# Kernel tuning notes

Measured on AMD Instinct MI355X. Metric: run time of the kernel, lower is better.

The kernel has to match this reference:

```python
import jax, jax.numpy as jnp
import numpy as np

N = 524288          # query points
N_COMP = 36         # sdf_n_comp
GRID = 512          # cubic grid resolution
SDF_DIM = 256
APP_DIM = 128
MAT_MODE = [(0, 1), (0, 2), (1, 2)]
VEC_MODE = [2, 1, 0]
PE_FREQS = (1.0, 2.0, 4.0)  # sdf_multires=3, log-sampled 2^0..2^2


def _pos_enc(x):
    # NeRF embedder, include_input=True: [x, sin(f x), cos(f x) per freq]
    outs = [x]
    for f in PE_FREQS:
        outs.append(jnp.sin(x * f))
        outs.append(jnp.cos(x * f))
    return jnp.concatenate(outs, axis=-1)  # (N, 21)


def _bilinear_plane(plane, gx, gy):
    # plane: (C, H, W); gx indexes W, gy indexes H; align_corners=True
    C, H, W = plane.shape
    px = (gx + 1.0) * 0.5 * (W - 1)
    py = (gy + 1.0) * 0.5 * (H - 1)
    x0 = jnp.clip(jnp.floor(px), 0, W - 2).astype(jnp.int32)
    y0 = jnp.clip(jnp.floor(py), 0, H - 2).astype(jnp.int32)
    x1, y1 = x0 + 1, y0 + 1
    wx = px - x0
    wy = py - y0
    f00 = plane[:, y0, x0]  # (C, N)
    f01 = plane[:, y0, x1]
    f10 = plane[:, y1, x0]
    f11 = plane[:, y1, x1]
    return (f00 * (1 - wx) + f01 * wx) * (1 - wy) + (f10 * (1 - wx) + f11 * wx) * wy


def _linear_line(line, g):
    # line: (C, L); g in [-1, 1]; align_corners=True
    C, L = line.shape
    p = (g + 1.0) * 0.5 * (L - 1)
    i0 = jnp.clip(jnp.floor(p), 0, L - 2).astype(jnp.int32)
    w = p - i0
    return line[:, i0] * (1 - w) + line[:, i0 + 1] * w  # (C, N)


def setup_inputs() -> dict:
    key = jax.random.key(0)
    ks = jax.random.split(key, 6)
    xyz = jax.random.uniform(ks[0], (N, 3), dtype=jnp.float32)  # points in aabb [0,1]^3
    planes = jax.random.normal(ks[1], (3, N_COMP, GRID, GRID), dtype=jnp.float32) * 0.1
    lines = jax.random.normal(ks[2], (3, N_COMP, GRID), dtype=jnp.float32) * 0.1
    in_ch = N_COMP * 3 + 21  # 129
    W1 = jax.random.normal(ks[3], (in_ch, SDF_DIM), dtype=jnp.float32) * (np.sqrt(2.0) / np.sqrt(SDF_DIM))
    b1 = jnp.zeros((SDF_DIM,), dtype=jnp.float32)
    W2 = jax.random.normal(ks[4], (SDF_DIM, 1 + APP_DIM), dtype=jnp.float32) * 0.0001 + np.sqrt(np.pi) / np.sqrt(SDF_DIM)
    b2 = jnp.full((1 + APP_DIM,), -0.2, dtype=jnp.float32)  # init_radius bias
    return {"xyz": xyz, "planes": planes, "lines": lines, "W1": W1, "b1": b1, "W2": W2, "b2": b2}


def reference(xyz, planes, lines, W1, b1, W2, b2):
    # contraction: normalize aabb [0,1]^3 -> [-1,1]
    xn = 2.0 * xyz - 1.0  # (N, 3)
    # sampling coords are detached in the original (coordinate_plane.detach())
    xs = jax.lax.stop_gradient(xn)
    feats = []
    for i in range(3):
        m0, m1 = MAT_MODE[i]
        pfeat = _bilinear_plane(planes[i], xs[:, m0], xs[:, m1])  # (C, N)
        lfeat = _linear_line(lines[i], xs[:, VEC_MODE[i]])        # (C, N)
        feats.append(pfeat * lfeat)
    feat = jnp.concatenate(feats, axis=0).T  # (N, 3C)
    pe = _pos_enc(xn)                         # (N, 21)
    h = jnp.concatenate([feat, pe], axis=-1)  # (N, 129)
    h = jax.nn.softplus(100.0 * (h @ W1 + b1)) / 100.0  # Softplus(beta=100)
    out = h @ W2 + b2  # (N, 1 + app_dim); out[..., :1] is the SDF
    return out
```

## Files before the change

kernel.cpp:

```cpp
#include <hip/hip_runtime.h>
#include <math.h>

typedef unsigned short u16;
typedef unsigned int u32;
typedef __attribute__((ext_vector_type(2))) u32 u32x2;
typedef __attribute__((ext_vector_type(8))) short short8;
typedef __attribute__((ext_vector_type(4))) float f32x4;
typedef __attribute__((ext_vector_type(2))) float f32x2;

#define OFF_LINES_T 62914560u
#define OFF_W1S     63037440u
#define OFF_W2S     63119360u
#define WS_NEEDED   63217664u

__device__ __forceinline__ float bf_lo(u32 u){ union{u32 i;float f;} v; v.i = u << 16; return v.f; }
__device__ __forceinline__ float bf_hi(u32 u){ union{u32 i;float f;} v; v.i = u & 0xffff0000u; return v.f; }
__device__ __forceinline__ u16 f2bf(float f){ union{float f;u32 i;} v; v.f=f; u32 i=v.i; return (u16)((i + 0x7fffu + ((i>>16)&1u)) >> 16); }
__device__ __forceinline__ u32 pack2bf(float lo, float hi){ return (u32)f2bf(lo) | ((u32)f2bf(hi)<<16); }
__device__ __forceinline__ u32 pack2bf_fast(float lo, float hi){
  return __builtin_amdgcn_perm(__float_as_uint(hi) + 0x8000u,
                               __float_as_uint(lo) + 0x8000u, 0x07060302u);
}
__device__ __forceinline__ u16 f2bf_fast(float f){ return (u16)((__float_as_uint(f) + 0x8000u) >> 16); }

__device__ __forceinline__ int map_k1(int kp){
  if (kp < 120){ int g = kp/40, r = kp - g*40; return (r<36) ? g*36 + r : -1; }
  if (kp < 141) return kp - 12;
  return -1;
}

#define NB_TP 3072
#define NB_TL 6
#define NB_W1 20
#define NB_W2 24
__global__ void k_pre(const float* __restrict__ planes, const float* __restrict__ lines,
                      const float* __restrict__ W1, const float* __restrict__ W2,
                      u16* __restrict__ pt, u16* __restrict__ lt,
                      u16* __restrict__ w1s, u16* __restrict__ w2s){
  const int b = blockIdx.x;
  const int tid = threadIdx.x;
  if (b < NB_TP){
    int t = b*256 + tid;
    int i = t >> 18;
    int yx = t & 262143;
    const float* src = planes + (size_t)i*9437184 + yx;
    uint4* dst = reinterpret_cast<uint4*>(pt + (size_t)t*40);
#pragma unroll
    for (int cc=0; cc<5; cc++){
      float v[8];
#pragma unroll
      for (int e=0;e<8;e++){
        int c = cc*8+e;
        v[e] = (c<36) ? src[(size_t)c*262144] : 0.f;
      }
      uint4 o; o.x=pack2bf(v[0],v[1]); o.y=pack2bf(v[2],v[3]); o.z=pack2bf(v[4],v[5]); o.w=pack2bf(v[6],v[7]);
      dst[cc]=o;
    }
  } else if (b < NB_TP+NB_TL){
    int t = (b-NB_TP)*256 + tid;
    int i = t >> 9, g = t & 511;
    const float* src = lines + (size_t)i*18432 + g;
    uint4* dst = reinterpret_cast<uint4*>(lt + (size_t)t*40);
#pragma unroll
    for (int cc=0; cc<5; cc++){
      float v[8];
#pragma unroll
      for (int e=0;e<8;e++){
        int c = cc*8+e;
        v[e] = (c<36) ? src[(size_t)c*512] : 0.f;
      }
      uint4 o; o.x=pack2bf(v[0],v[1]); o.y=pack2bf(v[2],v[3]); o.z=pack2bf(v[4],v[5]); o.w=pack2bf(v[6],v[7]);
      dst[cc]=o;
    }
  } else if (b < NB_TP+NB_TL+NB_W1){
    int t = (b-(NB_TP+NB_TL))*256 + tid;
    int lane = t & 63;
    int fid = t >> 6;
    int nt = fid/5, kt = fid - nt*5;
    int n = nt*16 + (lane & 15);
    int kb = kt*32 + (lane >> 4)*8;
    float v[8];
#pragma unroll
    for (int j=0;j<8;j++){ int k = map_k1(kb+j); v[j] = (k>=0) ? W1[k*256+n] : 0.f; }
    uint4 o; o.x=pack2bf(v[0],v[1]); o.y=pack2bf(v[2],v[3]); o.z=pack2bf(v[4],v[5]); o.w=pack2bf(v[6],v[7]);
    *reinterpret_cast<uint4*>(w1s + (size_t)t*8) = o;
  } else {
    int t = (b-(NB_TP+NB_TL+NB_W1))*256 + tid;
    int lane = t & 63;
    int fid = t >> 6;
    int kb = (fid & 7)*32 + (lane >> 4)*8;
    int n = (fid >> 3)*16 + (lane & 15);
    float v[8];
#pragma unroll
    for (int j=0;j<8;j++){ int k = kb+j; v[j] = (n<129) ? W2[k*129+n] : 0.f; }
    uint4 o; o.x=pack2bf(v[0],v[1]); o.y=pack2bf(v[2],v[3]); o.z=pack2bf(v[4],v[5]); o.w=pack2bf(v[6],v[7]);
    *reinterpret_cast<uint4*>(w2s + (size_t)t*8) = o;
  }
}

__device__ __forceinline__ f32x2 bfx2(u32 u){
  f32x2 r;
  r.x = __uint_as_float(u << 16);
  r.y = __uint_as_float(u & 0xffff0000u);
  return r;
}

__device__ __forceinline__ u32 blend2(u32 u00,u32 u01,u32 u10,u32 u11,u32 g0,u32 g1,
                                      float w00,float w01,float w10,float w11,
                                      float v0,float v1){
  f32x2 pf = bfx2(u00)*w00 + bfx2(u01)*w01 + bfx2(u10)*w10 + bfx2(u11)*w11;
  f32x2 lf = bfx2(g0)*v0 + bfx2(g1)*v1;
  f32x2 r  = pf*lf;
  return pack2bf_fast(r.x, r.y);
}

#define FSTRIDE 168
#define HSTRIDE 264

__global__ void __launch_bounds__(512, 4) k_main(
    const float* __restrict__ xyz, const u16* __restrict__ pt,
    const u16* __restrict__ lt, const u16* __restrict__ w1s,
    const u16* __restrict__ w2s, const float* __restrict__ b1,
    const float* __restrict__ b2, float* __restrict__ out)
{
  __shared__ u16 smem[64*HSTRIDE];
  const int tid = threadIdx.x;
  const int p = tid >> 3, q = tid & 7;
  const int gp = blockIdx.x*64 + p;
  const float u0 = xyz[gp*3], u1 = xyz[gp*3+1], u2 = xyz[gp*3+2];
  const float xn0 = 2.f*u0-1.f, xn1 = 2.f*u1-1.f, xn2 = 2.f*u2-1.f;

  if (q < 6){
    const int i = q >> 1, part = q & 1;
    float gxv, gyv, gzv;
    if      (i==0){ gxv=xn0; gyv=xn1; gzv=xn2; }
    else if (i==1){ gxv=xn0; gyv=xn2; gzv=xn1; }
    else          { gxv=xn1; gyv=xn2; gzv=xn0; }
    float px=(gxv+1.0f)*0.5f*511.0f, py=(gyv+1.0f)*0.5f*511.0f, pz=(gzv+1.0f)*0.5f*511.0f;
    float fx=fminf(fmaxf(floorf(px),0.f),510.f);
    float fy=fminf(fmaxf(floorf(py),0.f),510.f);
    float fz=fminf(fmaxf(floorf(pz),0.f),510.f);
    int ix=(int)fx, iy=(int)fy, iz=(int)fz;
    float wx=px-fx, wy=py-fy, wz=pz-fz;
    const float cwx = 1.f-wx, cwy = 1.f-wy;
    const float w00 = cwx*cwy, w01 = wx*cwy, w10 = cwx*wy, w11 = wx*wy;
    const float v0 = 1.f-wz, v1 = wz;
    const u16* base  = pt + (size_t)((i<<18)+(iy<<9)+ix)*40 + part*20;
    const u16* lbase = lt + (size_t)((i<<9)+iz)*40 + part*20;

    u32x2 A00[5],A01[5],A10[5],A11[5],E0[5],E1[5];
#pragma unroll
    for (int c=0; c<5; c++){
      A00[c] = *reinterpret_cast<const u32x2*>(base + c*4);
      A01[c] = *reinterpret_cast<const u32x2*>(base + 40 + c*4);
      A10[c] = *reinterpret_cast<const u32x2*>(base + 20480 + c*4);
      A11[c] = *reinterpret_cast<const u32x2*>(base + 20520 + c*4);
      E0[c]  = *reinterpret_cast<const u32x2*>(lbase + c*4);
      E1[c]  = *reinterpret_cast<const u32x2*>(lbase + 40 + c*4);
    }
    u16* dst = smem + p*FSTRIDE + i*40 + part*20;
#pragma unroll
    for (int c=0; c<5; c++){
      u32x2 o;
      o.x = blend2(A00[c].x,A01[c].x,A10[c].x,A11[c].x,E0[c].x,E1[c].x, w00,w01,w10,w11,v0,v1);
      o.y = blend2(A00[c].y,A01[c].y,A10[c].y,A11[c].y,E0[c].y,E1[c].y, w00,w01,w10,w11,v0,v1);
      *reinterpret_cast<u32x2*>(dst + c*4) = o;
    }
  } else if (q == 6){
    float v[20];
    v[0]=xn0; v[1]=xn1; v[2]=xn2;
    v[3]=__sinf(xn0);      v[4]=__sinf(xn1);      v[5]=__sinf(xn2);
    v[6]=__cosf(xn0);      v[7]=__cosf(xn1);      v[8]=__cosf(xn2);
    v[9]=__sinf(2.f*xn0);  v[10]=__sinf(2.f*xn1); v[11]=__sinf(2.f*xn2);
    v[12]=__cosf(2.f*xn0); v[13]=__cosf(2.f*xn1); v[14]=__cosf(2.f*xn2);
    v[15]=__sinf(4.f*xn0); v[16]=__sinf(4.f*xn1); v[17]=__sinf(4.f*xn2);
    v[18]=__cosf(4.f*xn0); v[19]=__cosf(4.f*xn1);
    u16* dst = smem + p*FSTRIDE + 120;
#pragma unroll
    for (int c=0; c<10; c++)
      *reinterpret_cast<u32*>(dst + c*2) = pack2bf_fast(v[c*2], v[c*2+1]);
  } else {
    u16* dst = smem + p*FSTRIDE + 140;
    *reinterpret_cast<u32*>(dst) = pack2bf_fast(__cosf(4.f*xn2), 0.f);
#pragma unroll
    for (int c=1; c<10; c++)
      *reinterpret_cast<u32*>(dst + c*2) = 0u;
  }
  __syncthreads();

  const int lane = tid & 63;
  const int w = tid >> 6;
  const int wm = w & 1, wn = w >> 1;
  const int lm = lane & 15;
  const int quad = lane >> 4;
  const f32x4 zero = {0.f,0.f,0.f,0.f};
  f32x4 acc1[2][4];
#pragma unroll
  for (int mt=0; mt<2; mt++)
#pragma unroll
    for (int nt=0; nt<4; nt++) acc1[mt][nt] = zero;

#pragma unroll
  for (int kt=0; kt<5; kt++){
    short8 a[2];
#pragma unroll
    for (int mt=0; mt<2; mt++)
      a[mt] = *reinterpret_cast<const short8*>(smem + ((wm*2+mt)*16 + lm)*FSTRIDE + kt*32 + quad*8);
    short8 b[4];
#pragma unroll
    for (int nt=0; nt<4; nt++)
      b[nt] = *reinterpret_cast<const short8*>(w1s + (size_t)(((wn*4+nt)*5 + kt)*64 + lane)*8);
#pragma unroll
    for (int mt=0; mt<2; mt++)
#pragma unroll
      for (int nt=0; nt<4; nt++)
        acc1[mt][nt] = __builtin_amdgcn_mfma_f32_16x16x32_bf16(a[mt], b[nt], acc1[mt][nt], 0,0,0);
  }
  __syncthreads();

#pragma unroll
  for (int nt=0; nt<4; nt++){
    int col = wn*64 + nt*16 + lm;
    float bias = b1[col];
#pragma unroll
    for (int mt=0; mt<2; mt++){
#pragma unroll
      for (int r=0; r<4; r++){
        float xv = acc1[mt][nt][r] + bias;
        float z = 100.f*xv;
        float y = (z > 15.f) ? xv : __logf(1.f + __expf(z))*0.01f;
        int row = (wm*2+mt)*16 + quad*4 + r;
        smem[row*HSTRIDE + col] = f2bf_fast(y);
      }
    }
  }
  __syncthreads();

  f32x4 acc2[2][3];
#pragma unroll
  for (int mt=0; mt<2; mt++)
#pragma unroll
    for (int nt=0; nt<3; nt++) acc2[mt][nt] = zero;

#pragma unroll
  for (int kt=0; kt<8; kt++){
    short8 a[2];
#pragma unroll
    for (int mt=0; mt<2; mt++)
      a[mt] = *reinterpret_cast<const short8*>(smem + ((wm*2+mt)*16 + lm)*HSTRIDE + kt*32 + quad*8);
    short8 b[3];
#pragma unroll
    for (int nt=0; nt<3; nt++){
      int ntg = wn*3 + nt;
      b[nt] = *reinterpret_cast<const short8*>(w2s + (size_t)((ntg*8 + kt)*64 + lane)*8);
    }
#pragma unroll
    for (int mt=0; mt<2; mt++)
#pragma unroll
      for (int nt=0; nt<3; nt++)
        acc2[mt][nt] = __builtin_amdgcn_mfma_f32_16x16x32_bf16(a[mt], b[nt], acc2[mt][nt], 0,0,0);
  }

#pragma unroll
  for (int nt=0; nt<3; nt++){
    int j = (wn*3 + nt)*16 + lm;
    if (j < 129){
      float bias = b2[j];
#pragma unroll
      for (int mt=0; mt<2; mt++){
#pragma unroll
        for (int r=0; r<4; r++){
          int row = (wm*2+mt)*16 + quad*4 + r;
          __builtin_nontemporal_store(acc2[mt][nt][r] + bias,
                                      &out[(size_t)(blockIdx.x*64 + row)*129 + j]);
        }
      }
    }
  }
}

extern "C" void kernel_launch(void* const* d_in, const int* in_sizes, int n_in,
                              void* d_out, int out_size, void* d_ws, size_t ws_size,
                              hipStream_t stream) {
  const float* xyz    = (const float*)d_in[0];
  const float* planes = (const float*)d_in[1];
  const float* lines  = (const float*)d_in[2];
  const float* W1     = (const float*)d_in[3];
  const float* b1     = (const float*)d_in[4];
  const float* W2     = (const float*)d_in[5];
  const float* b2     = (const float*)d_in[6];
  if (ws_size < (size_t)WS_NEEDED) return;

  u16* pt  = (u16*)((char*)d_ws);
  u16* lt  = (u16*)((char*)d_ws + OFF_LINES_T);
  u16* w1s = (u16*)((char*)d_ws + OFF_W1S);
  u16* w2s = (u16*)((char*)d_ws + OFF_W2S);

  k_pre<<<NB_TP+NB_TL+NB_W1+NB_W2, 256, 0, stream>>>(planes, lines, W1, W2, pt, lt, w1s, w2s);
  k_main<<<8192, 512, 0, stream>>>(xyz, pt, lt, w1s, w2s, b1, b2, (float*)d_out);
}
```

Before: 673.1 us.

## Raise occupancy to five blocks, widen gather loads, reuse accumulator registers

Measured after the change: 646.2 us. 4.0% less time.

```diff
diff --git a/kernel.cpp b/kernel.cpp
--- a/kernel.cpp
+++ b/kernel.cpp
@@ -117,7 +117,7 @@
 #define FSTRIDE 168
 #define HSTRIDE 264
 
-__global__ void __launch_bounds__(512, 4) k_main(
+__global__ void __launch_bounds__(512, 5) k_main(
     const float* __restrict__ xyz, const u16* __restrict__ pt,
     const u16* __restrict__ lt, const u16* __restrict__ w1s,
     const u16* __restrict__ w2s, const float* __restrict__ b1,
@@ -145,26 +145,26 @@
     const float cwx = 1.f-wx, cwy = 1.f-wy;
     const float w00 = cwx*cwy, w01 = wx*cwy, w10 = cwx*wy, w11 = wx*wy;
     const float v0 = 1.f-wz, v1 = wz;
-    const u16* base  = pt + (size_t)((i<<18)+(iy<<9)+ix)*40 + part*20;
-    const u16* lbase = lt + (size_t)((i<<9)+iz)*40 + part*20;
-
-    u32x2 A00[5],A01[5],A10[5],A11[5],E0[5],E1[5];
-#pragma unroll
-    for (int c=0; c<5; c++){
-      A00[c] = *reinterpret_cast<const u32x2*>(base + c*4);
-      A01[c] = *reinterpret_cast<const u32x2*>(base + 40 + c*4);
-      A10[c] = *reinterpret_cast<const u32x2*>(base + 20480 + c*4);
-      A11[c] = *reinterpret_cast<const u32x2*>(base + 20520 + c*4);
-      E0[c]  = *reinterpret_cast<const u32x2*>(lbase + c*4);
-      E1[c]  = *reinterpret_cast<const u32x2*>(lbase + 40 + c*4);
-    }
-    u16* dst = smem + p*FSTRIDE + i*40 + part*20;
-#pragma unroll
-    for (int c=0; c<5; c++){
-      u32x2 o;
-      o.x = blend2(A00[c].x,A01[c].x,A10[c].x,A11[c].x,E0[c].x,E1[c].x, w00,w01,w10,w11,v0,v1);
-      o.y = blend2(A00[c].y,A01[c].y,A10[c].y,A11[c].y,E0[c].y,E1[c].y, w00,w01,w10,w11,v0,v1);
-      *reinterpret_cast<u32x2*>(dst + c*4) = o;
+    const int nch = part ? 2 : 3;
+    const u16* tb = pt + (size_t)((i<<18)+(iy<<9)+ix)*40 + part*24;
+    const u16* lb = lt + (size_t)((i<<9)+iz)*40 + part*24;
+    u16* dst = smem + p*FSTRIDE + i*40 + part*24;
+#pragma unroll
+    for (int ch=0; ch<3; ch++){
+      if (ch < nch){
+        uint4 a00 = *reinterpret_cast<const uint4*>(tb + ch*8);
+        uint4 a01 = *reinterpret_cast<const uint4*>(tb + 40 + ch*8);
+        uint4 a10 = *reinterpret_cast<const uint4*>(tb + 20480 + ch*8);
+        uint4 a11 = *reinterpret_cast<const uint4*>(tb + 20520 + ch*8);
+        uint4 e0  = *reinterpret_cast<const uint4*>(lb + ch*8);
+        uint4 e1  = *reinterpret_cast<const uint4*>(lb + 40 + ch*8);
+        uint4 o;
+        o.x = blend2(a00.x,a01.x,a10.x,a11.x,e0.x,e1.x, w00,w01,w10,w11,v0,v1);
+        o.y = blend2(a00.y,a01.y,a10.y,a11.y,e0.y,e1.y, w00,w01,w10,w11,v0,v1);
+        o.z = blend2(a00.z,a01.z,a10.z,a11.z,e0.z,e1.z, w00,w01,w10,w11,v0,v1);
+        o.w = blend2(a00.w,a01.w,a10.w,a11.w,e0.w,e1.w, w00,w01,w10,w11,v0,v1);
+        *reinterpret_cast<uint4*>(dst + ch*8) = o;
+      }
     }
   } else if (q == 6){
     float v[20];
@@ -194,11 +194,11 @@
   const int lm = lane & 15;
   const int quad = lane >> 4;
   const f32x4 zero = {0.f,0.f,0.f,0.f};
-  f32x4 acc1[2][4];
+  f32x4 acc[2][4];
 #pragma unroll
   for (int mt=0; mt<2; mt++)
 #pragma unroll
-    for (int nt=0; nt<4; nt++) acc1[mt][nt] = zero;
+    for (int nt=0; nt<4; nt++) acc[mt][nt] = zero;
 
 #pragma unroll
   for (int kt=0; kt<5; kt++){
@@ -214,7 +214,7 @@
     for (int mt=0; mt<2; mt++)
 #pragma unroll
       for (int nt=0; nt<4; nt++)
-        acc1[mt][nt] = __builtin_amdgcn_mfma_f32_16x16x32_bf16(a[mt], b[nt], acc1[mt][nt], 0,0,0);
+        acc[mt][nt] = __builtin_amdgcn_mfma_f32_16x16x32_bf16(a[mt], b[nt], acc[mt][nt], 0,0,0);
   }
   __syncthreads();
 
@@ -226,7 +226,7 @@
     for (int mt=0; mt<2; mt++){
 #pragma unroll
       for (int r=0; r<4; r++){
-        float xv = acc1[mt][nt][r] + bias;
+        float xv = acc[mt][nt][r] + bias;
         float z = 100.f*xv;
         float y = (z > 15.f) ? xv : __logf(1.f + __expf(z))*0.01f;
         int row = (wm*2+mt)*16 + quad*4 + r;
@@ -236,11 +236,10 @@
   }
   __syncthreads();
 
-  f32x4 acc2[2][3];
 #pragma unroll
   for (int mt=0; mt<2; mt++)
 #pragma unroll
-    for (int nt=0; nt<3; nt++) acc2[mt][nt] = zero;
+    for (int nt=0; nt<3; nt++) acc[mt][nt] = zero;
 
 #pragma unroll
   for (int kt=0; kt<8; kt++){
@@ -258,7 +257,7 @@
     for (int mt=0; mt<2; mt++)
 #pragma unroll
       for (int nt=0; nt<3; nt++)
-        acc2[mt][nt] = __builtin_amdgcn_mfma_f32_16x16x32_bf16(a[mt], b[nt], acc2[mt][nt], 0,0,0);
+        acc[mt][nt] = __builtin_amdgcn_mfma_f32_16x16x32_bf16(a[mt], b[nt], acc[mt][nt], 0,0,0);
   }
 
 #pragma unroll
@@ -271,8 +270,7 @@
 #pragma unroll
         for (int r=0; r<4; r++){
           int row = (wm*2+mt)*16 + quad*4 + r;
-          __builtin_nontemporal_store(acc2[mt][nt][r] + bias,
-                                      &out[(size_t)(blockIdx.x*64 + row)*129 + j]);
+          out[(size_t)(blockIdx.x*64 + row)*129 + j] = acc[mt][nt][r] + bias;
         }
       }
     }
```
